# Performance work log

Measured on AMD Instinct MI355X. Metric: run time of the kernel, lower is better.

## Reference

```python
import jax, jax.numpy as jnp
import numpy as np

B, T, C = 32, 4096, 256


def setup_inputs() -> dict:
    key = jax.random.key(0)
    ks = jax.random.split(key, 10)
    s = lambda *sh: 0.05
    return {
        "gru_output": jax.random.normal(ks[0], (B, T, C), jnp.float32),
        "intensity_curves": jax.random.uniform(ks[1], (B, T), jnp.float32),
        "W1": jax.random.normal(ks[2], (C, 128), jnp.float32) * 0.05,
        "b1": jnp.zeros((128,), jnp.float32),
        "W2": jax.random.normal(ks[3], (128, 64), jnp.float32) * 0.05,
        "b2": jnp.zeros((64,), jnp.float32),
        "W3": jax.random.normal(ks[4], (64, 4), jnp.float32) * 0.05,
        "b3": jnp.zeros((4,), jnp.float32),
        "conv_w": jax.random.normal(ks[5], (1, C, 3), jnp.float32) * 0.05,  # OIH
        "conv_b": jnp.zeros((1,), jnp.float32),
    }


def reference(gru_output, intensity_curves, W1, b1, W2, b2, W3, b3, conv_w, conv_b):
    Bb, Tt, Cc = gru_output.shape
    # per-timestep phase classifier MLP + softmax -> (B,T,4)
    h = jax.nn.relu(gru_output @ W1 + b1)
    h = jax.nn.relu(h @ W2 + b2)
    phase_probs = jax.nn.softmax(h @ W3 + b3, axis=-1)
    # transition scores: Conv1d(C->1,k=3,pad=1) + sigmoid -> (B,T)
    x = jnp.transpose(gru_output, (0, 2, 1))  # (B,C,T)
    ts = jax.lax.conv_general_dilated(x, conv_w, (1,), 'SAME',
                                      dimension_numbers=('NCH', 'OIH', 'NCH'))
    transition_scores = jax.nn.sigmoid(ts[:, 0, :] + conv_b[0])  # (B,T)
    # run-length segments: new segment when dominant phase changes or transition>0.7
    dom = jnp.argmax(phase_probs, axis=-1)  # (B,T) int
    change = (dom[:, 1:] != dom[:, :-1]) | (transition_scores[:, 1:] > 0.7)
    change = jnp.concatenate([jnp.zeros((Bb, 1), bool), change], axis=1)
    seg = jnp.cumsum(change.astype(jnp.int32), axis=1)  # (B,T) segment id per step
    gseg = (seg + jnp.arange(Bb, dtype=jnp.int32)[:, None] * Tt).reshape(-1)
    nseg = Bb * Tt
    cnt = jax.ops.segment_sum(jnp.ones((nseg,), jnp.float32)[: gseg.shape[0]] * 0 + 1.0,
                              gseg, num_segments=nseg)
    sum_int = jax.ops.segment_sum(intensity_curves.reshape(-1), gseg, num_segments=nseg)
    conf_t = jnp.take_along_axis(phase_probs, dom[..., None], axis=2)[..., 0]  # (B,T)
    sum_conf = jax.ops.segment_sum(conf_t.reshape(-1), gseg, num_segments=nseg)
    denom = jnp.maximum(cnt, 1.0)
    mean_int = (sum_int / denom)[gseg].reshape(Bb, Tt)   # segment-mean intensity per step
    mean_conf = (sum_conf / denom)[gseg].reshape(Bb, Tt)  # segment-mean confidence per step
    return phase_probs, transition_scores, seg, mean_int, mean_conf
```

## Files before the change

### kernel.cpp

```cpp
#include <hip/hip_runtime.h>

#define B_ 32
#define T_ 4096
#define C_ 256
#define R_ (B_*T_)
#define H1_ 128
#define H2_ 64

#define TB 64

#define PROBS_OFF 0
#define TS_OFF  (R_*4)
#define SEG_OFF (TS_OFF + R_)
#define MI_OFF  (SEG_OFF + R_)
#define MC_OFF  (MI_OFF + R_)

#define XS_OFF  0
#define XS_P    268
#define H1S_OFF 0
#define H1S_P   132
#define W2S_OFF 8448
#define W1S_OFF 17152
#define SMEMF   19200

__device__ __forceinline__ void fma4(float4& a, float s, const float4& b) {
  a.x = fmaf(s, b.x, a.x); a.y = fmaf(s, b.y, a.y);
  a.z = fmaf(s, b.z, a.z); a.w = fmaf(s, b.w, a.w);
}

__global__ __launch_bounds__(256, 2) void mlp_conv_kernel(
    const float* __restrict__ X, const float* __restrict__ W1, const float* __restrict__ b1,
    const float* __restrict__ W2, const float* __restrict__ b2,
    const float* __restrict__ W3, const float* __restrict__ b3,
    const float* __restrict__ CW, const float* __restrict__ CB,
    float* __restrict__ out)
{
  __shared__ float sm[SMEMF];
  const int tid  = threadIdx.x;
  const int l    = tid & 63;
  const int w    = tid >> 6;
  const int row0 = blockIdx.x * TB;

  float4 st0 = ((const float4*)W1)[tid];
  float4 st1 = ((const float4*)W1)[tid + 256];

  #pragma unroll
  for (int i2 = 0; i2 < 16; ++i2) {
    int g = tid + 256 * i2;
    int r = g >> 6, m = g & 63;
    float4 v = *(const float4*)&X[(size_t)(row0 + r) * C_ + m * 4];
    *(float4*)&sm[XS_OFF + r * XS_P + m * 4] = v;
  }
  __syncthreads();

  #pragma unroll
  for (int half = 0; half < 2; ++half) {
    const int rowi = half * 32 + w * 8 + (l & 7);
    const int p = l >> 3;
    const int grow = row0 + rowi;
    const int tb = grow & (T_ - 1);
    float s = 0.f;
    #pragma unroll
    for (int cc = 0; cc < 8; ++cc) {
      const int c = p * 32 + cc * 4;
      float4 x0 = *(const float4*)&sm[XS_OFF + rowi * XS_P + c];
      float4 xm, xp;
      if (tb == 0)             xm = make_float4(0.f, 0.f, 0.f, 0.f);
      else if (rowi >= 1)      xm = *(const float4*)&sm[XS_OFF + (rowi - 1) * XS_P + c];
      else                     xm = *(const float4*)&X[(size_t)(grow - 1) * C_ + c];
      if (tb == T_ - 1)        xp = make_float4(0.f, 0.f, 0.f, 0.f);
      else if (rowi + 1 < TB)  xp = *(const float4*)&sm[XS_OFF + (rowi + 1) * XS_P + c];
      else                     xp = *(const float4*)&X[(size_t)(grow + 1) * C_ + c];
      float4 wa = *(const float4*)&CW[c * 3 + 0];
      float4 wb = *(const float4*)&CW[c * 3 + 4];
      float4 wc = *(const float4*)&CW[c * 3 + 8];
      s += xm.x * wa.x + x0.x * wa.y + xp.x * wa.z;
      s += xm.y * wa.w + x0.y * wb.x + xp.y * wb.y;
      s += xm.z * wb.z + x0.z * wb.w + xp.z * wc.x;
      s += xm.w * wc.y + x0.w * wc.z + xp.w * wc.w;
    }
    s += __shfl_xor(s, 8);
    s += __shfl_xor(s, 16);
    s += __shfl_xor(s, 32);
    if (p == 0) out[TS_OFF + grow] = 1.f / (1.f + expf(-(s + CB[0])));
  }

  const int rt = tid >> 5, ct = tid & 31;
  const int rb = rt * 8;
  float4 acc[8];
  #pragma unroll
  for (int r = 0; r < 8; ++r) acc[r] = make_float4(0.f, 0.f, 0.f, 0.f);

  for (int kc = 0; kc < 16; ++kc) {
    *(float4*)&sm[W1S_OFF + tid * 4]         = st0;
    *(float4*)&sm[W1S_OFF + (tid + 256) * 4] = st1;
    __syncthreads();
    if (kc + 1 < 16) {
      const float* wp = W1 + (size_t)(kc + 1) * 2048;
      st0 = ((const float4*)wp)[tid];
      st1 = ((const float4*)wp)[tid + 256];
    } else {
      st0 = ((const float4*)W2)[tid];
      st1 = ((const float4*)W2)[tid + 256];
    }
    #pragma unroll
    for (int k4 = 0; k4 < 4; ++k4) {
      const int kb = kc * 16 + k4 * 4;
      float4 a0 = *(const float4*)&sm[XS_OFF + (rb + 0) * XS_P + kb];
      float4 a1 = *(const float4*)&sm[XS_OFF + (rb + 1) * XS_P + kb];
      float4 a2 = *(const float4*)&sm[XS_OFF + (rb + 2) * XS_P + kb];
      float4 a3 = *(const float4*)&sm[XS_OFF + (rb + 3) * XS_P + kb];
      float4 a4 = *(const float4*)&sm[XS_OFF + (rb + 4) * XS_P + kb];
      float4 a5 = *(const float4*)&sm[XS_OFF + (rb + 5) * XS_P + kb];
      float4 a6 = *(const float4*)&sm[XS_OFF + (rb + 6) * XS_P + kb];
      float4 a7 = *(const float4*)&sm[XS_OFF + (rb + 7) * XS_P + kb];
      float4 q0 = *(const float4*)&sm[W1S_OFF + (k4 * 4 + 0) * H1_ + ct * 4];
      float4 q1 = *(const float4*)&sm[W1S_OFF + (k4 * 4 + 1) * H1_ + ct * 4];
      float4 q2 = *(const float4*)&sm[W1S_OFF + (k4 * 4 + 2) * H1_ + ct * 4];
      float4 q3 = *(const float4*)&sm[W1S_OFF + (k4 * 4 + 3) * H1_ + ct * 4];
      fma4(acc[0], a0.x, q0); fma4(acc[0], a0.y, q1); fma4(acc[0], a0.z, q2); fma4(acc[0], a0.w, q3);
      fma4(acc[1], a1.x, q0); fma4(acc[1], a1.y, q1); fma4(acc[1], a1.z, q2); fma4(acc[1], a1.w, q3);
      fma4(acc[2], a2.x, q0); fma4(acc[2], a2.y, q1); fma4(acc[2], a2.z, q2); fma4(acc[2], a2.w, q3);
      fma4(acc[3], a3.x, q0); fma4(acc[3], a3.y, q1); fma4(acc[3], a3.z, q2); fma4(acc[3], a3.w, q3);
      fma4(acc[4], a4.x, q0); fma4(acc[4], a4.y, q1); fma4(acc[4], a4.z, q2); fma4(acc[4], a4.w, q3);
      fma4(acc[5], a5.x, q0); fma4(acc[5], a5.y, q1); fma4(acc[5], a5.z, q2); fma4(acc[5], a5.w, q3);
      fma4(acc[6], a6.x, q0); fma4(acc[6], a6.y, q1); fma4(acc[6], a6.z, q2); fma4(acc[6], a6.w, q3);
      fma4(acc[7], a7.x, q0); fma4(acc[7], a7.y, q1); fma4(acc[7], a7.z, q2); fma4(acc[7], a7.w, q3);
    }
    __syncthreads();
  }

  const int rt2 = tid >> 4, ct2 = tid & 15;
  float4 w2r[6];
  #pragma unroll
  for (int i = 0; i < 6; ++i) w2r[i] = ((const float4*)W2)[tid + 512 + 256 * i];
  float4 w30 = ((const float4*)W3)[ct2 * 4 + 0];
  float4 w31 = ((const float4*)W3)[ct2 * 4 + 1];
  float4 w32 = ((const float4*)W3)[ct2 * 4 + 2];
  float4 w33 = ((const float4*)W3)[ct2 * 4 + 3];
  float4 b3v = *(const float4*)&b3[0];

  {
    float4 bb = ((const float4*)b1)[ct];
    #pragma unroll
    for (int r = 0; r < 8; ++r) {
      float4 h = acc[r];
      h.x = fmaxf(h.x + bb.x, 0.f); h.y = fmaxf(h.y + bb.y, 0.f);
      h.z = fmaxf(h.z + bb.z, 0.f); h.w = fmaxf(h.w + bb.w, 0.f);
      *(float4*)&sm[H1S_OFF + (rb + r) * H1S_P + ct * 4] = h;
    }
  }
  *(float4*)&sm[W2S_OFF + tid * 4]         = st0;
  *(float4*)&sm[W2S_OFF + (tid + 256) * 4] = st1;
  #pragma unroll
  for (int i = 0; i < 6; ++i)
    *(float4*)&sm[W2S_OFF + (tid + 512 + 256 * i) * 4] = w2r[i];
  __syncthreads();

  float4 acc2[4];
  #pragma unroll
  for (int j = 0; j < 4; ++j) acc2[j] = make_float4(0.f, 0.f, 0.f, 0.f);
  #pragma unroll 4
  for (int k4 = 0; k4 < 32; ++k4) {
    float4 a0 = *(const float4*)&sm[H1S_OFF + (rt2 * 4 + 0) * H1S_P + k4 * 4];
    float4 a1 = *(const float4*)&sm[H1S_OFF + (rt2 * 4 + 1) * H1S_P + k4 * 4];
    float4 a2 = *(const float4*)&sm[H1S_OFF + (rt2 * 4 + 2) * H1S_P + k4 * 4];
    float4 a3 = *(const float4*)&sm[H1S_OFF + (rt2 * 4 + 3) * H1S_P + k4 * 4];
    float4 q0 = *(const float4*)&sm[W2S_OFF + (k4 * 4 + 0) * H2_ + ct2 * 4];
    float4 q1 = *(const float4*)&sm[W2S_OFF + (k4 * 4 + 1) * H2_ + ct2 * 4];
    float4 q2 = *(const float4*)&sm[W2S_OFF + (k4 * 4 + 2) * H2_ + ct2 * 4];
    float4 q3 = *(const float4*)&sm[W2S_OFF + (k4 * 4 + 3) * H2_ + ct2 * 4];
    fma4(acc2[0], a0.x, q0); fma4(acc2[0], a0.y, q1); fma4(acc2[0], a0.z, q2); fma4(acc2[0], a0.w, q3);
    fma4(acc2[1], a1.x, q0); fma4(acc2[1], a1.y, q1); fma4(acc2[1], a1.z, q2); fma4(acc2[1], a1.w, q3);
    fma4(acc2[2], a2.x, q0); fma4(acc2[2], a2.y, q1); fma4(acc2[2], a2.z, q2); fma4(acc2[2], a2.w, q3);
    fma4(acc2[3], a3.x, q0); fma4(acc2[3], a3.y, q1); fma4(acc2[3], a3.z, q2); fma4(acc2[3], a3.w, q3);
  }

  float4 L[4];
  {
    float4 bb = ((const float4*)b2)[ct2];
    #pragma unroll
    for (int r = 0; r < 4; ++r) {
      float4 h = acc2[r];
      h.x = fmaxf(h.x + bb.x, 0.f); h.y = fmaxf(h.y + bb.y, 0.f);
      h.z = fmaxf(h.z + bb.z, 0.f); h.w = fmaxf(h.w + bb.w, 0.f);
      float4 t = make_float4(0.f, 0.f, 0.f, 0.f);
      fma4(t, h.x, w30); fma4(t, h.y, w31); fma4(t, h.z, w32); fma4(t, h.w, w33);
      L[r] = t;
    }
  }
  #pragma unroll
  for (int d = 1; d < 16; d <<= 1) {
    #pragma unroll
    for (int r = 0; r < 4; ++r) {
      L[r].x += __shfl_xor(L[r].x, d);
      L[r].y += __shfl_xor(L[r].y, d);
      L[r].z += __shfl_xor(L[r].z, d);
      L[r].w += __shfl_xor(L[r].w, d);
    }
  }

  if (ct2 < 4) {
    float4 Lv = L[ct2];
    const int grow = row0 + rt2 * 4 + ct2;
    Lv.x += b3v.x; Lv.y += b3v.y; Lv.z += b3v.z; Lv.w += b3v.w;
    float mx = fmaxf(fmaxf(Lv.x, Lv.y), fmaxf(Lv.z, Lv.w));
    float e0 = expf(Lv.x - mx), e1 = expf(Lv.y - mx), e2 = expf(Lv.z - mx), e3 = expf(Lv.w - mx);
    float inv = 1.f / ((e0 + e1) + (e2 + e3));
    float p0 = e0 * inv, p1 = e1 * inv, p2 = e2 * inv, p3 = e3 * inv;
    *(float4*)&out[PROBS_OFF + (size_t)grow * 4] = make_float4(p0, p1, p2, p3);
    int dom = 0; float pm = p0;
    if (p1 > pm) { pm = p1; dom = 1; }
    if (p2 > pm) { pm = p2; dom = 2; }
    if (p3 > pm) { pm = p3; dom = 3; }
    out[MI_OFF + grow] = (float)dom;
    out[MC_OFF + grow] = pm;
  }
}

__global__ __launch_bounds__(1024, 1) void seg_kernel(
    const float* __restrict__ inten, float* __restrict__ out)
{
  __shared__ float scnt[T_], ssi[T_], ssc[T_];
  __shared__ int wtot[16], wexcl[16];
  const int tid = threadIdx.x;
  const int lane = tid & 63, wid = tid >> 6;
  const size_t base = (size_t)blockIdx.x * T_;
  const float* tsS = out + TS_OFF;
  float* segO = out + SEG_OFF;
  float* miO  = out + MI_OFF;
  float* mcO  = out + MC_OFF;
  const int t4 = tid * 4;

  float4 dv = *(const float4*)&miO[base + t4];
  float4 tv = *(const float4*)&tsS[base + t4];
  float4 iv = *(const float4*)&inten[base + t4];
  float4 cv = *(const float4*)&mcO[base + t4];
  float pd = (tid == 0) ? 0.f : miO[base + t4 - 1];

  for (int i = tid; i < T_; i += 1024) { scnt[i] = 0.f; ssi[i] = 0.f; ssc[i] = 0.f; }

  int c0 = (t4 == 0) ? 0 : (((dv.x != pd)   || (tv.x > 0.7f)) ? 1 : 0);
  int c1 = ((dv.y != dv.x) || (tv.y > 0.7f)) ? 1 : 0;
  int c2 = ((dv.z != dv.y) || (tv.z > 0.7f)) ? 1 : 0;
  int c3 = ((dv.w != dv.z) || (tv.w > 0.7f)) ? 1 : 0;
  int l0 = c0, l1 = c0 + c1, l2 = l1 + c2, l3 = l2 + c3;
  const int tsum = l3;

  int v = tsum;
  #pragma unroll
  for (int d = 1; d < 64; d <<= 1) {
    int o = __shfl_up(v, (unsigned)d);
    if (lane >= d) v += o;
  }
  if (lane == 63) wtot[wid] = v;
  __syncthreads();
  if (tid < 16) {
    int x = wtot[tid];
    int xx = x;
    #pragma unroll
    for (int d = 1; d < 16; d <<= 1) {
      int o = __shfl_up(xx, (unsigned)d);
      if (tid >= d) xx += o;
    }
    wexcl[tid] = xx - x;
  }
  __syncthreads();
  const int texcl = wexcl[wid] + (v - tsum);
  const int s0 = texcl + l0, s1 = texcl + l1, s2 = texcl + l2, s3 = texcl + l3;

  {
    int cur = s0; float aI = iv.x, aC = cv.x, aN = 1.f;
    if (s1 == cur) { aI += iv.y; aC += cv.y; aN += 1.f; }
    else { atomicAdd(&ssi[cur], aI); atomicAdd(&ssc[cur], aC); atomicAdd(&scnt[cur], aN);
           cur = s1; aI = iv.y; aC = cv.y; aN = 1.f; }
    if (s2 == cur) { aI += iv.z; aC += cv.z; aN += 1.f; }
    else { atomicAdd(&ssi[cur], aI); atomicAdd(&ssc[cur], aC); atomicAdd(&scnt[cur], aN);
           cur = s2; aI = iv.z; aC = cv.z; aN = 1.f; }
    if (s3 == cur) { aI += iv.w; aC += cv.w; aN += 1.f; }
    else { atomicAdd(&ssi[cur], aI); atomicAdd(&ssc[cur], aC); atomicAdd(&scnt[cur], aN);
           cur = s3; aI = iv.w; aC = cv.w; aN = 1.f; }
    atomicAdd(&ssi[cur], aI); atomicAdd(&ssc[cur], aC); atomicAdd(&scnt[cur], aN);
  }
  __syncthreads();

  float n0 = scnt[s0], n1 = scnt[s1], n2 = scnt[s2], n3 = scnt[s3];
  float4 m4, q4, g4;
  m4.x = ssi[s0] / n0; m4.y = ssi[s1] / n1; m4.z = ssi[s2] / n2; m4.w = ssi[s3] / n3;
  q4.x = ssc[s0] / n0; q4.y = ssc[s1] / n1; q4.z = ssc[s2] / n2; q4.w = ssc[s3] / n3;
  g4.x = (float)s0; g4.y = (float)s1; g4.z = (float)s2; g4.w = (float)s3;
  *(float4*)&segO[base + t4] = g4;
  *(float4*)&miO[base + t4]  = m4;
  *(float4*)&mcO[base + t4]  = q4;
}

extern "C" void kernel_launch(void* const* d_in, const int* in_sizes, int n_in,
                              void* d_out, int out_size, void* d_ws, size_t ws_size,
                              hipStream_t stream) {
  (void)in_sizes; (void)n_in; (void)out_size; (void)d_ws; (void)ws_size;
  const float* X   = (const float*)d_in[0];
  const float* INT = (const float*)d_in[1];
  const float* W1  = (const float*)d_in[2];
  const float* B1  = (const float*)d_in[3];
  const float* W2  = (const float*)d_in[4];
  const float* B2  = (const float*)d_in[5];
  const float* W3  = (const float*)d_in[6];
  const float* B3  = (const float*)d_in[7];
  const float* CW  = (const float*)d_in[8];
  const float* CB  = (const float*)d_in[9];
  float* out = (float*)d_out;

  hipLaunchKernelGGL(mlp_conv_kernel, dim3(R_ / TB), dim3(256), 0, stream,
                     X, W1, B1, W2, B2, W3, B3, CW, CB, out);
  hipLaunchKernelGGL(seg_kernel, dim3(B_), dim3(1024), 0, stream, INT, out);
}
```

Before: 179.5 us.

## Shrink shared memory by streaming X k-chunks and splitting W2 staging

The full 64-row X tile is no longer held in shared memory for the first GEMM. The conv now stages X in two 32-row halves, and the layer-1 GEMM streams 16-column X chunks into a small padded buffer alongside the W1 chunk, prefetched one step ahead. W2 is staged in two halves with a sync between them, which brings shared memory down from about 77KB to about 50KB, and launch bounds are raised to 3 blocks per CU to increase occupancy. The cost is that each X row is read from global memory twice (once for the conv, once for the GEMM), plus extra barriers and register pressure under the tighter launch bound.

```diff
diff --git a/kernel.cpp b/kernel.cpp
--- a/kernel.cpp
+++ b/kernel.cpp
@@ -16,19 +16,21 @@
 #define MC_OFF  (MI_OFF + R_)
 
 #define XS_OFF  0
-#define XS_P    268
+#define XS_P    260
 #define H1S_OFF 0
 #define H1S_P   132
+#define W1S_OFF 8448
+#define AC_OFF  10496
+#define AC_P    20
 #define W2S_OFF 8448
-#define W1S_OFF 17152
-#define SMEMF   19200
+#define SMEMF   12544
 
 __device__ __forceinline__ void fma4(float4& a, float s, const float4& b) {
   a.x = fmaf(s, b.x, a.x); a.y = fmaf(s, b.y, a.y);
   a.z = fmaf(s, b.z, a.z); a.w = fmaf(s, b.w, a.w);
 }
 
-__global__ __launch_bounds__(256, 2) void mlp_conv_kernel(
+__global__ __launch_bounds__(256, 3) void mlp_conv_kernel(
     const float* __restrict__ X, const float* __restrict__ W1, const float* __restrict__ b1,
     const float* __restrict__ W2, const float* __restrict__ b2,
     const float* __restrict__ W3, const float* __restrict__ b3,
@@ -40,24 +42,26 @@
   const int l    = tid & 63;
   const int w    = tid >> 6;
   const int row0 = blockIdx.x * TB;
+  const float4* Xf4 = (const float4*)X;
 
   float4 st0 = ((const float4*)W1)[tid];
   float4 st1 = ((const float4*)W1)[tid + 256];
-
-  #pragma unroll
-  for (int i2 = 0; i2 < 16; ++i2) {
-    int g = tid + 256 * i2;
-    int r = g >> 6, m = g & 63;
-    float4 v = *(const float4*)&X[(size_t)(row0 + r) * C_ + m * 4];
-    *(float4*)&sm[XS_OFF + r * XS_P + m * 4] = v;
-  }
-  __syncthreads();
+  float4 sa0 = Xf4[(size_t)(row0 + (tid >> 2)) * 64 + (tid & 3)];
 
   #pragma unroll
   for (int half = 0; half < 2; ++half) {
-    const int rowi = half * 32 + w * 8 + (l & 7);
+    if (half) __syncthreads();
+    #pragma unroll
+    for (int i2 = 0; i2 < 8; ++i2) {
+      int g = tid + 256 * i2;
+      int r = g >> 6, m = g & 63;
+      float4 v = *(const float4*)&X[(size_t)(row0 + half * 32 + r) * C_ + m * 4];
+      *(float4*)&sm[XS_OFF + r * XS_P + m * 4] = v;
+    }
+    __syncthreads();
+    const int rowi = w * 8 + (l & 7);
     const int p = l >> 3;
-    const int grow = row0 + rowi;
+    const int grow = row0 + half * 32 + rowi;
     const int tb = grow & (T_ - 1);
     float s = 0.f;
     #pragma unroll
@@ -65,12 +69,12 @@
       const int c = p * 32 + cc * 4;
       float4 x0 = *(const float4*)&sm[XS_OFF + rowi * XS_P + c];
       float4 xm, xp;
-      if (tb == 0)             xm = make_float4(0.f, 0.f, 0.f, 0.f);
-      else if (rowi >= 1)      xm = *(const float4*)&sm[XS_OFF + (rowi - 1) * XS_P + c];
-      else                     xm = *(const float4*)&X[(size_t)(grow - 1) * C_ + c];
-      if (tb == T_ - 1)        xp = make_float4(0.f, 0.f, 0.f, 0.f);
-      else if (rowi + 1 < TB)  xp = *(const float4*)&sm[XS_OFF + (rowi + 1) * XS_P + c];
-      else                     xp = *(const float4*)&X[(size_t)(grow + 1) * C_ + c];
+      if (tb == 0)            xm = make_float4(0.f, 0.f, 0.f, 0.f);
+      else if (rowi >= 1)     xm = *(const float4*)&sm[XS_OFF + (rowi - 1) * XS_P + c];
+      else                    xm = *(const float4*)&X[(size_t)(grow - 1) * C_ + c];
+      if (tb == T_ - 1)       xp = make_float4(0.f, 0.f, 0.f, 0.f);
+      else if (rowi + 1 < 32) xp = *(const float4*)&sm[XS_OFF + (rowi + 1) * XS_P + c];
+      else                    xp = *(const float4*)&X[(size_t)(grow + 1) * C_ + c];
       float4 wa = *(const float4*)&CW[c * 3 + 0];
       float4 wb = *(const float4*)&CW[c * 3 + 4];
       float4 wc = *(const float4*)&CW[c * 3 + 8];
@@ -84,9 +88,12 @@
     s += __shfl_xor(s, 32);
     if (p == 0) out[TS_OFF + grow] = 1.f / (1.f + expf(-(s + CB[0])));
   }
+  __syncthreads();
 
   const int rt = tid >> 5, ct = tid & 31;
   const int rb = rt * 8;
+  const int acq = (tid >> 2) * AC_P + (tid & 3) * 4;
+  float4 w2x;
   float4 acc[8];
   #pragma unroll
   for (int r = 0; r < 8; ++r) acc[r] = make_float4(0.f, 0.f, 0.f, 0.f);
@@ -94,26 +101,29 @@
   for (int kc = 0; kc < 16; ++kc) {
     *(float4*)&sm[W1S_OFF + tid * 4]         = st0;
     *(float4*)&sm[W1S_OFF + (tid + 256) * 4] = st1;
+    *(float4*)&sm[AC_OFF + acq]              = sa0;
     __syncthreads();
     if (kc + 1 < 16) {
       const float* wp = W1 + (size_t)(kc + 1) * 2048;
       st0 = ((const float4*)wp)[tid];
       st1 = ((const float4*)wp)[tid + 256];
+      sa0 = Xf4[(size_t)(row0 + (tid >> 2)) * 64 + (kc + 1) * 4 + (tid & 3)];
     } else {
       st0 = ((const float4*)W2)[tid];
       st1 = ((const float4*)W2)[tid + 256];
+      sa0 = ((const float4*)W2)[tid + 512];
+      w2x = ((const float4*)W2)[tid + 768];
     }
     #pragma unroll
     for (int k4 = 0; k4 < 4; ++k4) {
-      const int kb = kc * 16 + k4 * 4;
-      float4 a0 = *(const float4*)&sm[XS_OFF + (rb + 0) * XS_P + kb];
-      float4 a1 = *(const float4*)&sm[XS_OFF + (rb + 1) * XS_P + kb];
-      float4 a2 = *(const float4*)&sm[XS_OFF + (rb + 2) * XS_P + kb];
-      float4 a3 = *(const float4*)&sm[XS_OFF + (rb + 3) * XS_P + kb];
-      float4 a4 = *(const float4*)&sm[XS_OFF + (rb + 4) * XS_P + kb];
-      float4 a5 = *(const float4*)&sm[XS_OFF + (rb + 5) * XS_P + kb];
-      float4 a6 = *(const float4*)&sm[XS_OFF + (rb + 6) * XS_P + kb];
-      float4 a7 = *(const float4*)&sm[XS_OFF + (rb + 7) * XS_P + kb];
+      float4 a0 = *(const float4*)&sm[AC_OFF + (rb + 0) * AC_P + k4 * 4];
+      float4 a1 = *(const float4*)&sm[AC_OFF + (rb + 1) * AC_P + k4 * 4];
+      float4 a2 = *(const float4*)&sm[AC_OFF + (rb + 2) * AC_P + k4 * 4];
+      float4 a3 = *(const float4*)&sm[AC_OFF + (rb + 3) * AC_P + k4 * 4];
+      float4 a4 = *(const float4*)&sm[AC_OFF + (rb + 4) * AC_P + k4 * 4];
+      float4 a5 = *(const float4*)&sm[AC_OFF + (rb + 5) * AC_P + k4 * 4];
+      float4 a6 = *(const float4*)&sm[AC_OFF + (rb + 6) * AC_P + k4 * 4];
+      float4 a7 = *(const float4*)&sm[AC_OFF + (rb + 7) * AC_P + k4 * 4];
       float4 q0 = *(const float4*)&sm[W1S_OFF + (k4 * 4 + 0) * H1_ + ct * 4];
       float4 q1 = *(const float4*)&sm[W1S_OFF + (k4 * 4 + 1) * H1_ + ct * 4];
       float4 q2 = *(const float4*)&sm[W1S_OFF + (k4 * 4 + 2) * H1_ + ct * 4];
@@ -131,9 +141,6 @@
   }
 
   const int rt2 = tid >> 4, ct2 = tid & 15;
-  float4 w2r[6];
-  #pragma unroll
-  for (int i = 0; i < 6; ++i) w2r[i] = ((const float4*)W2)[tid + 512 + 256 * i];
   float4 w30 = ((const float4*)W3)[ct2 * 4 + 0];
   float4 w31 = ((const float4*)W3)[ct2 * 4 + 1];
   float4 w32 = ((const float4*)W3)[ct2 * 4 + 2];
@@ -152,16 +159,20 @@
   }
   *(float4*)&sm[W2S_OFF + tid * 4]         = st0;
   *(float4*)&sm[W2S_OFF + (tid + 256) * 4] = st1;
-  #pragma unroll
-  for (int i = 0; i < 6; ++i)
-    *(float4*)&sm[W2S_OFF + (tid + 512 + 256 * i) * 4] = w2r[i];
-  __syncthreads();
+  *(float4*)&sm[W2S_OFF + (tid + 512) * 4] = sa0;
+  *(float4*)&sm[W2S_OFF + (tid + 768) * 4] = w2x;
+  __syncthreads();
+
+  st0 = ((const float4*)W2)[tid + 1024];
+  st1 = ((const float4*)W2)[tid + 1280];
+  sa0 = ((const float4*)W2)[tid + 1536];
+  w2x = ((const float4*)W2)[tid + 1792];
 
   float4 acc2[4];
   #pragma unroll
   for (int j = 0; j < 4; ++j) acc2[j] = make_float4(0.f, 0.f, 0.f, 0.f);
   #pragma unroll 4
-  for (int k4 = 0; k4 < 32; ++k4) {
+  for (int k4 = 0; k4 < 16; ++k4) {
     float4 a0 = *(const float4*)&sm[H1S_OFF + (rt2 * 4 + 0) * H1S_P + k4 * 4];
     float4 a1 = *(const float4*)&sm[H1S_OFF + (rt2 * 4 + 1) * H1S_P + k4 * 4];
     float4 a2 = *(const float4*)&sm[H1S_OFF + (rt2 * 4 + 2) * H1S_P + k4 * 4];
@@ -170,6 +181,27 @@
     float4 q1 = *(const float4*)&sm[W2S_OFF + (k4 * 4 + 1) * H2_ + ct2 * 4];
     float4 q2 = *(const float4*)&sm[W2S_OFF + (k4 * 4 + 2) * H2_ + ct2 * 4];
     float4 q3 = *(const float4*)&sm[W2S_OFF + (k4 * 4 + 3) * H2_ + ct2 * 4];
+    fma4(acc2[0], a0.x, q0); fma4(acc2[0], a0.y, q1); fma4(acc2[0], a0.z, q2); fma4(acc2[0], a0.w, q3);
+    fma4(acc2[1], a1.x, q0); fma4(acc2[1], a1.y, q1); fma4(acc2[1], a1.z, q2); fma4(acc2[1], a1.w, q3);
+    fma4(acc2[2], a2.x, q0); fma4(acc2[2], a2.y, q1); fma4(acc2[2], a2.z, q2); fma4(acc2[2], a2.w, q3);
+    fma4(acc2[3], a3.x, q0); fma4(acc2[3], a3.y, q1); fma4(acc2[3], a3.z, q2); fma4(acc2[3], a3.w, q3);
+  }
+  __syncthreads();
+  *(float4*)&sm[W2S_OFF + tid * 4]         = st0;
+  *(float4*)&sm[W2S_OFF + (tid + 256) * 4] = st1;
+  *(float4*)&sm[W2S_OFF + (tid + 512) * 4] = sa0;
+  *(float4*)&sm[W2S_OFF + (tid + 768) * 4] = w2x;
+  __syncthreads();
+  #pragma unroll 4
+  for (int k4 = 16; k4 < 32; ++k4) {
+    float4 a0 = *(const float4*)&sm[H1S_OFF + (rt2 * 4 + 0) * H1S_P + k4 * 4];
+    float4 a1 = *(const float4*)&sm[H1S_OFF + (rt2 * 4 + 1) * H1S_P + k4 * 4];
+    float4 a2 = *(const float4*)&sm[H1S_OFF + (rt2 * 4 + 2) * H1S_P + k4 * 4];
+    float4 a3 = *(const float4*)&sm[H1S_OFF + (rt2 * 4 + 3) * H1S_P + k4 * 4];
+    float4 q0 = *(const float4*)&sm[W2S_OFF + ((k4 - 16) * 4 + 0) * H2_ + ct2 * 4];
+    float4 q1 = *(const float4*)&sm[W2S_OFF + ((k4 - 16) * 4 + 1) * H2_ + ct2 * 4];
+    float4 q2 = *(const float4*)&sm[W2S_OFF + ((k4 - 16) * 4 + 2) * H2_ + ct2 * 4];
+    float4 q3 = *(const float4*)&sm[W2S_OFF + ((k4 - 16) * 4 + 3) * H2_ + ct2 * 4];
     fma4(acc2[0], a0.x, q0); fma4(acc2[0], a0.y, q1); fma4(acc2[0], a0.z, q2); fma4(acc2[0], a0.w, q3);
     fma4(acc2[1], a1.x, q0); fma4(acc2[1], a1.y, q1); fma4(acc2[1], a1.z, q2); fma4(acc2[1], a1.w, q3);
     fma4(acc2[2], a2.x, q0); fma4(acc2[2], a2.y, q1); fma4(acc2[2], a2.z, q2); fma4(acc2[2], a2.w, q3);
```

New measurement: 231.1 us. +28.7%, slower.

## Drop LDS staging of X and weights; stream operands from global with register double-buffering

Applied to the files above, without the earlier changes.

The kernel no longer stages the X tile and the W1/W2 weight chunks through shared memory. The conv and the first GEMM read X directly from global memory, and both GEMMs read weights straight from global/L2 with software-pipelined register double buffers. Only the hidden activations H1 stay in LDS. This shrinks LDS use and removes most barriers, and launch bounds are raised to 3 blocks per CU for more occupancy. The cost is redundant global/L2 traffic: each X row is re-read by many threads and weights are fetched per thread, so it relies on cache hit rates and may pressure registers under the tighter bound.

```diff
diff --git a/kernel.cpp b/kernel.cpp
--- a/kernel.cpp
+++ b/kernel.cpp
@@ -15,20 +15,15 @@
 #define MI_OFF  (SEG_OFF + R_)
 #define MC_OFF  (MI_OFF + R_)
 
-#define XS_OFF  0
-#define XS_P    268
-#define H1S_OFF 0
 #define H1S_P   132
-#define W2S_OFF 8448
-#define W1S_OFF 17152
-#define SMEMF   19200
+#define SMEMF   (64 * H1S_P)
 
 __device__ __forceinline__ void fma4(float4& a, float s, const float4& b) {
   a.x = fmaf(s, b.x, a.x); a.y = fmaf(s, b.y, a.y);
   a.z = fmaf(s, b.z, a.z); a.w = fmaf(s, b.w, a.w);
 }
 
-__global__ __launch_bounds__(256, 2) void mlp_conv_kernel(
+__global__ __launch_bounds__(256, 3) void mlp_conv_kernel(
     const float* __restrict__ X, const float* __restrict__ W1, const float* __restrict__ b1,
     const float* __restrict__ W2, const float* __restrict__ b2,
     const float* __restrict__ W3, const float* __restrict__ b3,
@@ -41,36 +36,23 @@
   const int w    = tid >> 6;
   const int row0 = blockIdx.x * TB;
 
-  float4 st0 = ((const float4*)W1)[tid];
-  float4 st1 = ((const float4*)W1)[tid + 256];
-
-  #pragma unroll
-  for (int i2 = 0; i2 < 16; ++i2) {
-    int g = tid + 256 * i2;
-    int r = g >> 6, m = g & 63;
-    float4 v = *(const float4*)&X[(size_t)(row0 + r) * C_ + m * 4];
-    *(float4*)&sm[XS_OFF + r * XS_P + m * 4] = v;
-  }
-  __syncthreads();
-
   #pragma unroll
   for (int half = 0; half < 2; ++half) {
     const int rowi = half * 32 + w * 8 + (l & 7);
     const int p = l >> 3;
     const int grow = row0 + rowi;
     const int tb = grow & (T_ - 1);
+    const float* x0p = X + (size_t)grow * C_;
     float s = 0.f;
     #pragma unroll
     for (int cc = 0; cc < 8; ++cc) {
       const int c = p * 32 + cc * 4;
-      float4 x0 = *(const float4*)&sm[XS_OFF + rowi * XS_P + c];
+      float4 x0 = *(const float4*)&x0p[c];
       float4 xm, xp;
-      if (tb == 0)             xm = make_float4(0.f, 0.f, 0.f, 0.f);
-      else if (rowi >= 1)      xm = *(const float4*)&sm[XS_OFF + (rowi - 1) * XS_P + c];
-      else                     xm = *(const float4*)&X[(size_t)(grow - 1) * C_ + c];
-      if (tb == T_ - 1)        xp = make_float4(0.f, 0.f, 0.f, 0.f);
-      else if (rowi + 1 < TB)  xp = *(const float4*)&sm[XS_OFF + (rowi + 1) * XS_P + c];
-      else                     xp = *(const float4*)&X[(size_t)(grow + 1) * C_ + c];
+      if (tb == 0)        xm = make_float4(0.f, 0.f, 0.f, 0.f);
+      else                xm = *(const float4*)&x0p[c - C_];
+      if (tb == T_ - 1)   xp = make_float4(0.f, 0.f, 0.f, 0.f);
+      else                xp = *(const float4*)&x0p[c + C_];
       float4 wa = *(const float4*)&CW[c * 3 + 0];
       float4 wb = *(const float4*)&CW[c * 3 + 4];
       float4 wc = *(const float4*)&CW[c * 3 + 8];
@@ -87,103 +69,99 @@
 
   const int rt = tid >> 5, ct = tid & 31;
   const int rb = rt * 8;
+  const float* xb = X + (size_t)(row0 + rb) * C_;
+  const float* wb1 = W1 + ct * 4;
   float4 acc[8];
   #pragma unroll
   for (int r = 0; r < 8; ++r) acc[r] = make_float4(0.f, 0.f, 0.f, 0.f);
-
-  for (int kc = 0; kc < 16; ++kc) {
-    *(float4*)&sm[W1S_OFF + tid * 4]         = st0;
-    *(float4*)&sm[W1S_OFF + (tid + 256) * 4] = st1;
-    __syncthreads();
-    if (kc + 1 < 16) {
-      const float* wp = W1 + (size_t)(kc + 1) * 2048;
-      st0 = ((const float4*)wp)[tid];
-      st1 = ((const float4*)wp)[tid + 256];
-    } else {
-      st0 = ((const float4*)W2)[tid];
-      st1 = ((const float4*)W2)[tid + 256];
-    }
-    #pragma unroll
-    for (int k4 = 0; k4 < 4; ++k4) {
-      const int kb = kc * 16 + k4 * 4;
-      float4 a0 = *(const float4*)&sm[XS_OFF + (rb + 0) * XS_P + kb];
-      float4 a1 = *(const float4*)&sm[XS_OFF + (rb + 1) * XS_P + kb];
-      float4 a2 = *(const float4*)&sm[XS_OFF + (rb + 2) * XS_P + kb];
-      float4 a3 = *(const float4*)&sm[XS_OFF + (rb + 3) * XS_P + kb];
-      float4 a4 = *(const float4*)&sm[XS_OFF + (rb + 4) * XS_P + kb];
-      float4 a5 = *(const float4*)&sm[XS_OFF + (rb + 5) * XS_P + kb];
-      float4 a6 = *(const float4*)&sm[XS_OFF + (rb + 6) * XS_P + kb];
-      float4 a7 = *(const float4*)&sm[XS_OFF + (rb + 7) * XS_P + kb];
-      float4 q0 = *(const float4*)&sm[W1S_OFF + (k4 * 4 + 0) * H1_ + ct * 4];
-      float4 q1 = *(const float4*)&sm[W1S_OFF + (k4 * 4 + 1) * H1_ + ct * 4];
-      float4 q2 = *(const float4*)&sm[W1S_OFF + (k4 * 4 + 2) * H1_ + ct * 4];
-      float4 q3 = *(const float4*)&sm[W1S_OFF + (k4 * 4 + 3) * H1_ + ct * 4];
-      fma4(acc[0], a0.x, q0); fma4(acc[0], a0.y, q1); fma4(acc[0], a0.z, q2); fma4(acc[0], a0.w, q3);
-      fma4(acc[1], a1.x, q0); fma4(acc[1], a1.y, q1); fma4(acc[1], a1.z, q2); fma4(acc[1], a1.w, q3);
-      fma4(acc[2], a2.x, q0); fma4(acc[2], a2.y, q1); fma4(acc[2], a2.z, q2); fma4(acc[2], a2.w, q3);
-      fma4(acc[3], a3.x, q0); fma4(acc[3], a3.y, q1); fma4(acc[3], a3.z, q2); fma4(acc[3], a3.w, q3);
-      fma4(acc[4], a4.x, q0); fma4(acc[4], a4.y, q1); fma4(acc[4], a4.z, q2); fma4(acc[4], a4.w, q3);
-      fma4(acc[5], a5.x, q0); fma4(acc[5], a5.y, q1); fma4(acc[5], a5.z, q2); fma4(acc[5], a5.w, q3);
-      fma4(acc[6], a6.x, q0); fma4(acc[6], a6.y, q1); fma4(acc[6], a6.z, q2); fma4(acc[6], a6.w, q3);
-      fma4(acc[7], a7.x, q0); fma4(acc[7], a7.y, q1); fma4(acc[7], a7.z, q2); fma4(acc[7], a7.w, q3);
-    }
-    __syncthreads();
-  }
+  {
+    float4 A0[8], A1[8], B0[4], B1[4];
+    #pragma unroll
+    for (int r = 0; r < 8; ++r) A0[r] = *(const float4*)&xb[r * C_];
+    #pragma unroll
+    for (int j = 0; j < 4; ++j) B0[j] = *(const float4*)&wb1[(size_t)j * H1_];
+
+    #define G1STEP(Ac, Bc, An, Bn, kb, pf)                                        \
+      {                                                                           \
+        if (pf) {                                                                 \
+          _Pragma("unroll")                                                       \
+          for (int r = 0; r < 8; ++r) An[r] = *(const float4*)&xb[r * C_ + (kb) + 4]; \
+          _Pragma("unroll")                                                       \
+          for (int j = 0; j < 4; ++j) Bn[j] = *(const float4*)&wb1[(size_t)((kb) + 4 + j) * H1_]; \
+        }                                                                         \
+        _Pragma("unroll")                                                         \
+        for (int r = 0; r < 8; ++r) {                                             \
+          fma4(acc[r], Ac[r].x, Bc[0]); fma4(acc[r], Ac[r].y, Bc[1]);             \
+          fma4(acc[r], Ac[r].z, Bc[2]); fma4(acc[r], Ac[r].w, Bc[3]);             \
+        }                                                                         \
+      }
+
+    for (int k4 = 0; k4 < 64; k4 += 2) {
+      G1STEP(A0, B0, A1, B1, k4 * 4, 1)
+      G1STEP(A1, B1, A0, B0, k4 * 4 + 4, (k4 + 2 < 64))
+    }
+    #undef G1STEP
+  }
+
+  {
+    float4 bb = ((const float4*)b1)[ct];
+    #pragma unroll
+    for (int r = 0; r < 8; ++r) {
+      float4 h = acc[r];
+      h.x = fmaxf(h.x + bb.x, 0.f); h.y = fmaxf(h.y + bb.y, 0.f);
+      h.z = fmaxf(h.z + bb.z, 0.f); h.w = fmaxf(h.w + bb.w, 0.f);
+      *(float4*)&sm[(rb + r) * H1S_P + ct * 4] = h;
+    }
+  }
+  __syncthreads();
 
   const int rt2 = tid >> 4, ct2 = tid & 15;
-  float4 w2r[6];
-  #pragma unroll
-  for (int i = 0; i < 6; ++i) w2r[i] = ((const float4*)W2)[tid + 512 + 256 * i];
   float4 w30 = ((const float4*)W3)[ct2 * 4 + 0];
   float4 w31 = ((const float4*)W3)[ct2 * 4 + 1];
   float4 w32 = ((const float4*)W3)[ct2 * 4 + 2];
   float4 w33 = ((const float4*)W3)[ct2 * 4 + 3];
+  float4 b2v = ((const float4*)b2)[ct2];
   float4 b3v = *(const float4*)&b3[0];
-
-  {
-    float4 bb = ((const float4*)b1)[ct];
-    #pragma unroll
-    for (int r = 0; r < 8; ++r) {
-      float4 h = acc[r];
-      h.x = fmaxf(h.x + bb.x, 0.f); h.y = fmaxf(h.y + bb.y, 0.f);
-      h.z = fmaxf(h.z + bb.z, 0.f); h.w = fmaxf(h.w + bb.w, 0.f);
-      *(float4*)&sm[H1S_OFF + (rb + r) * H1S_P + ct * 4] = h;
-    }
-  }
-  *(float4*)&sm[W2S_OFF + tid * 4]         = st0;
-  *(float4*)&sm[W2S_OFF + (tid + 256) * 4] = st1;
-  #pragma unroll
-  for (int i = 0; i < 6; ++i)
-    *(float4*)&sm[W2S_OFF + (tid + 512 + 256 * i) * 4] = w2r[i];
-  __syncthreads();
-
+  const float* w2b = W2 + ct2 * 4;
   float4 acc2[4];
   #pragma unroll
   for (int j = 0; j < 4; ++j) acc2[j] = make_float4(0.f, 0.f, 0.f, 0.f);
-  #pragma unroll 4
-  for (int k4 = 0; k4 < 32; ++k4) {
-    float4 a0 = *(const float4*)&sm[H1S_OFF + (rt2 * 4 + 0) * H1S_P + k4 * 4];
-    float4 a1 = *(const float4*)&sm[H1S_OFF + (rt2 * 4 + 1) * H1S_P + k4 * 4];
-    float4 a2 = *(const float4*)&sm[H1S_OFF + (rt2 * 4 + 2) * H1S_P + k4 * 4];
-    float4 a3 = *(const float4*)&sm[H1S_OFF + (rt2 * 4 + 3) * H1S_P + k4 * 4];
-    float4 q0 = *(const float4*)&sm[W2S_OFF + (k4 * 4 + 0) * H2_ + ct2 * 4];
-    float4 q1 = *(const float4*)&sm[W2S_OFF + (k4 * 4 + 1) * H2_ + ct2 * 4];
-    float4 q2 = *(const float4*)&sm[W2S_OFF + (k4 * 4 + 2) * H2_ + ct2 * 4];
-    float4 q3 = *(const float4*)&sm[W2S_OFF + (k4 * 4 + 3) * H2_ + ct2 * 4];
-    fma4(acc2[0], a0.x, q0); fma4(acc2[0], a0.y, q1); fma4(acc2[0], a0.z, q2); fma4(acc2[0], a0.w, q3);
-    fma4(acc2[1], a1.x, q0); fma4(acc2[1], a1.y, q1); fma4(acc2[1], a1.z, q2); fma4(acc2[1], a1.w, q3);
-    fma4(acc2[2], a2.x, q0); fma4(acc2[2], a2.y, q1); fma4(acc2[2], a2.z, q2); fma4(acc2[2], a2.w, q3);
-    fma4(acc2[3], a3.x, q0); fma4(acc2[3], a3.y, q1); fma4(acc2[3], a3.z, q2); fma4(acc2[3], a3.w, q3);
+  {
+    float4 A0[4], A1[4], B0[4], B1[4];
+    #pragma unroll
+    for (int r = 0; r < 4; ++r) A0[r] = *(const float4*)&sm[(rt2 * 4 + r) * H1S_P];
+    #pragma unroll
+    for (int j = 0; j < 4; ++j) B0[j] = *(const float4*)&w2b[(size_t)j * H2_];
+
+    #define G2STEP(Ac, Bc, An, Bn, kb, pf)                                        \
+      {                                                                           \
+        if (pf) {                                                                 \
+          _Pragma("unroll")                                                       \
+          for (int r = 0; r < 4; ++r) An[r] = *(const float4*)&sm[(rt2 * 4 + r) * H1S_P + (kb) + 4]; \
+          _Pragma("unroll")                                                       \
+          for (int j = 0; j < 4; ++j) Bn[j] = *(const float4*)&w2b[(size_t)((kb) + 4 + j) * H2_]; \
+        }                                                                         \
+        _Pragma("unroll")                                                         \
+        for (int r = 0; r < 4; ++r) {                                             \
+          fma4(acc2[r], Ac[r].x, Bc[0]); fma4(acc2[r], Ac[r].y, Bc[1]);           \
+          fma4(acc2[r], Ac[r].z, Bc[2]); fma4(acc2[r], Ac[r].w, Bc[3]);           \
+        }                                                                         \
+      }
+
+    for (int k4 = 0; k4 < 32; k4 += 2) {
+      G2STEP(A0, B0, A1, B1, k4 * 4, 1)
+      G2STEP(A1, B1, A0, B0, k4 * 4 + 4, (k4 + 2 < 32))
+    }
+    #undef G2STEP
   }
 
   float4 L[4];
   {
-    float4 bb = ((const float4*)b2)[ct2];
     #pragma unroll
     for (int r = 0; r < 4; ++r) {
       float4 h = acc2[r];
-      h.x = fmaxf(h.x + bb.x, 0.f); h.y = fmaxf(h.y + bb.y, 0.f);
-      h.z = fmaxf(h.z + bb.z, 0.f); h.w = fmaxf(h.w + bb.w, 0.f);
+      h.x = fmaxf(h.x + b2v.x, 0.f); h.y = fmaxf(h.y + b2v.y, 0.f);
+      h.z = fmaxf(h.z + b2v.z, 0.f); h.w = fmaxf(h.w + b2v.w, 0.f);
       float4 t = make_float4(0.f, 0.f, 0.f, 0.f);
       fma4(t, h.x, w30); fma4(t, h.y, w31); fma4(t, h.z, w32); fma4(t, h.w, w33);
       L[r] = t;
```

Measured after the change: 511.4 us, median of 2. +184.8%, slower.

## Double-buffer W1 chunks in LDS to halve barriers in first GEMM

Applied to the files above, without the earlier changes.

Replaces the single W1 staging buffer, which took two barriers per 16-row chunk, with two 8-row ping-pong buffers that are written while the other is being consumed, so each 8-row chunk needs one barrier. The first W1 chunk is stored before the conv stage so it overlaps that work. The X tile row pitch is also reduced from 268 to 260 floats, which changes the LDS bank pattern. W2 staging is moved entirely after the GEMM loop. Smaller chunks mean more loop iterations and possibly different bank conflicts in the X reads.

```diff
diff --git a/kernel.cpp b/kernel.cpp
--- a/kernel.cpp
+++ b/kernel.cpp
@@ -16,17 +16,44 @@
 #define MC_OFF  (MI_OFF + R_)
 
 #define XS_OFF  0
-#define XS_P    268
+#define XS_P    260
 #define H1S_OFF 0
 #define H1S_P   132
 #define W2S_OFF 8448
-#define W1S_OFF 17152
-#define SMEMF   19200
+#define W1B0    16640
+#define W1B1    17664
+#define SMEMF   18688
 
 __device__ __forceinline__ void fma4(float4& a, float s, const float4& b) {
   a.x = fmaf(s, b.x, a.x); a.y = fmaf(s, b.y, a.y);
   a.z = fmaf(s, b.z, a.z); a.w = fmaf(s, b.w, a.w);
 }
+
+#define G1CHUNK(BOFF, CB)                                                      \
+  _Pragma("unroll")                                                            \
+  for (int k4 = 0; k4 < 2; ++k4) {                                            \
+    const int colb = (CB) + k4 * 4;                                           \
+    float4 a0 = *(const float4*)&sm[XS_OFF + (rb + 0) * XS_P + colb];         \
+    float4 a1 = *(const float4*)&sm[XS_OFF + (rb + 1) * XS_P + colb];         \
+    float4 a2 = *(const float4*)&sm[XS_OFF + (rb + 2) * XS_P + colb];         \
+    float4 a3 = *(const float4*)&sm[XS_OFF + (rb + 3) * XS_P + colb];         \
+    float4 a4 = *(const float4*)&sm[XS_OFF + (rb + 4) * XS_P + colb];         \
+    float4 a5 = *(const float4*)&sm[XS_OFF + (rb + 5) * XS_P + colb];         \
+    float4 a6 = *(const float4*)&sm[XS_OFF + (rb + 6) * XS_P + colb];         \
+    float4 a7 = *(const float4*)&sm[XS_OFF + (rb + 7) * XS_P + colb];         \
+    float4 q0 = *(const float4*)&sm[(BOFF) + (k4 * 4 + 0) * H1_ + ct * 4];    \
+    float4 q1 = *(const float4*)&sm[(BOFF) + (k4 * 4 + 1) * H1_ + ct * 4];    \
+    float4 q2 = *(const float4*)&sm[(BOFF) + (k4 * 4 + 2) * H1_ + ct * 4];    \
+    float4 q3 = *(const float4*)&sm[(BOFF) + (k4 * 4 + 3) * H1_ + ct * 4];    \
+    fma4(acc[0], a0.x, q0); fma4(acc[0], a0.y, q1); fma4(acc[0], a0.z, q2); fma4(acc[0], a0.w, q3); \
+    fma4(acc[1], a1.x, q0); fma4(acc[1], a1.y, q1); fma4(acc[1], a1.z, q2); fma4(acc[1], a1.w, q3); \
+    fma4(acc[2], a2.x, q0); fma4(acc[2], a2.y, q1); fma4(acc[2], a2.z, q2); fma4(acc[2], a2.w, q3); \
+    fma4(acc[3], a3.x, q0); fma4(acc[3], a3.y, q1); fma4(acc[3], a3.z, q2); fma4(acc[3], a3.w, q3); \
+    fma4(acc[4], a4.x, q0); fma4(acc[4], a4.y, q1); fma4(acc[4], a4.z, q2); fma4(acc[4], a4.w, q3); \
+    fma4(acc[5], a5.x, q0); fma4(acc[5], a5.y, q1); fma4(acc[5], a5.z, q2); fma4(acc[5], a5.w, q3); \
+    fma4(acc[6], a6.x, q0); fma4(acc[6], a6.y, q1); fma4(acc[6], a6.z, q2); fma4(acc[6], a6.w, q3); \
+    fma4(acc[7], a7.x, q0); fma4(acc[7], a7.y, q1); fma4(acc[7], a7.z, q2); fma4(acc[7], a7.w, q3); \
+  }
 
 __global__ __launch_bounds__(256, 2) void mlp_conv_kernel(
     const float* __restrict__ X, const float* __restrict__ W1, const float* __restrict__ b1,
@@ -41,8 +68,7 @@
   const int w    = tid >> 6;
   const int row0 = blockIdx.x * TB;
 
-  float4 st0 = ((const float4*)W1)[tid];
-  float4 st1 = ((const float4*)W1)[tid + 256];
+  float4 st = ((const float4*)W1)[tid];
 
   #pragma unroll
   for (int i2 = 0; i2 < 16; ++i2) {
@@ -52,6 +78,9 @@
     *(float4*)&sm[XS_OFF + r * XS_P + m * 4] = v;
   }
   __syncthreads();
+
+  *(float4*)&sm[W1B0 + tid * 4] = st;
+  st = ((const float4*)W1)[256 + tid];
 
   #pragma unroll
   for (int half = 0; half < 2; ++half) {
@@ -84,6 +113,7 @@
     s += __shfl_xor(s, 32);
     if (p == 0) out[TS_OFF + grow] = 1.f / (1.f + expf(-(s + CB[0])));
   }
+  __syncthreads();
 
   const int rt = tid >> 5, ct = tid & 31;
   const int rb = rt * 8;
@@ -91,53 +121,29 @@
   #pragma unroll
   for (int r = 0; r < 8; ++r) acc[r] = make_float4(0.f, 0.f, 0.f, 0.f);
 
-  for (int kc = 0; kc < 16; ++kc) {
-    *(float4*)&sm[W1S_OFF + tid * 4]         = st0;
-    *(float4*)&sm[W1S_OFF + (tid + 256) * 4] = st1;
+  #pragma unroll 1
+  for (int c = 0; c < 32; c += 2) {
+    G1CHUNK(W1B0, c * 8)
+    *(float4*)&sm[W1B1 + tid * 4] = st;
+    if (c + 2 < 32) st = ((const float4*)W1)[(c + 2) * 256 + tid];
     __syncthreads();
-    if (kc + 1 < 16) {
-      const float* wp = W1 + (size_t)(kc + 1) * 2048;
-      st0 = ((const float4*)wp)[tid];
-      st1 = ((const float4*)wp)[tid + 256];
-    } else {
-      st0 = ((const float4*)W2)[tid];
-      st1 = ((const float4*)W2)[tid + 256];
-    }
-    #pragma unroll
-    for (int k4 = 0; k4 < 4; ++k4) {
-      const int kb = kc * 16 + k4 * 4;
-      float4 a0 = *(const float4*)&sm[XS_OFF + (rb + 0) * XS_P + kb];
-      float4 a1 = *(const float4*)&sm[XS_OFF + (rb + 1) * XS_P + kb];
-      float4 a2 = *(const float4*)&sm[XS_OFF + (rb + 2) * XS_P + kb];
-      float4 a3 = *(const float4*)&sm[XS_OFF + (rb + 3) * XS_P + kb];
-      float4 a4 = *(const float4*)&sm[XS_OFF + (rb + 4) * XS_P + kb];
-      float4 a5 = *(const float4*)&sm[XS_OFF + (rb + 5) * XS_P + kb];
-      float4 a6 = *(const float4*)&sm[XS_OFF + (rb + 6) * XS_P + kb];
-      float4 a7 = *(const float4*)&sm[XS_OFF + (rb + 7) * XS_P + kb];
-      float4 q0 = *(const float4*)&sm[W1S_OFF + (k4 * 4 + 0) * H1_ + ct * 4];
-      float4 q1 = *(const float4*)&sm[W1S_OFF + (k4 * 4 + 1) * H1_ + ct * 4];
-      float4 q2 = *(const float4*)&sm[W1S_OFF + (k4 * 4 + 2) * H1_ + ct * 4];
-      float4 q3 = *(const float4*)&sm[W1S_OFF + (k4 * 4 + 3) * H1_ + ct * 4];
-      fma4(acc[0], a0.x, q0); fma4(acc[0], a0.y, q1); fma4(acc[0], a0.z, q2); fma4(acc[0], a0.w, q3);
-      fma4(acc[1], a1.x, q0); fma4(acc[1], a1.y, q1); fma4(acc[1], a1.z, q2); fma4(acc[1], a1.w, q3);
-      fma4(acc[2], a2.x, q0); fma4(acc[2], a2.y, q1); fma4(acc[2], a2.z, q2); fma4(acc[2], a2.w, q3);
-      fma4(acc[3], a3.x, q0); fma4(acc[3], a3.y, q1); fma4(acc[3], a3.z, q2); fma4(acc[3], a3.w, q3);
-      fma4(acc[4], a4.x, q0); fma4(acc[4], a4.y, q1); fma4(acc[4], a4.z, q2); fma4(acc[4], a4.w, q3);
-      fma4(acc[5], a5.x, q0); fma4(acc[5], a5.y, q1); fma4(acc[5], a5.z, q2); fma4(acc[5], a5.w, q3);
-      fma4(acc[6], a6.x, q0); fma4(acc[6], a6.y, q1); fma4(acc[6], a6.z, q2); fma4(acc[6], a6.w, q3);
-      fma4(acc[7], a7.x, q0); fma4(acc[7], a7.y, q1); fma4(acc[7], a7.z, q2); fma4(acc[7], a7.w, q3);
+    G1CHUNK(W1B1, c * 8 + 8)
+    if (c + 2 < 32) {
+      *(float4*)&sm[W1B0 + tid * 4] = st;
+      st = ((const float4*)W1)[(c + 3) * 256 + tid];
     }
     __syncthreads();
   }
 
   const int rt2 = tid >> 4, ct2 = tid & 15;
-  float4 w2r[6];
-  #pragma unroll
-  for (int i = 0; i < 6; ++i) w2r[i] = ((const float4*)W2)[tid + 512 + 256 * i];
+  float4 w2q[8];
+  #pragma unroll
+  for (int i = 0; i < 8; ++i) w2q[i] = ((const float4*)W2)[tid + 256 * i];
   float4 w30 = ((const float4*)W3)[ct2 * 4 + 0];
   float4 w31 = ((const float4*)W3)[ct2 * 4 + 1];
   float4 w32 = ((const float4*)W3)[ct2 * 4 + 2];
   float4 w33 = ((const float4*)W3)[ct2 * 4 + 3];
+  float4 b2v = ((const float4*)b2)[ct2];
   float4 b3v = *(const float4*)&b3[0];
 
   {
@@ -150,11 +156,9 @@
       *(float4*)&sm[H1S_OFF + (rb + r) * H1S_P + ct * 4] = h;
     }
   }
-  *(float4*)&sm[W2S_OFF + tid * 4]         = st0;
-  *(float4*)&sm[W2S_OFF + (tid + 256) * 4] = st1;
-  #pragma unroll
-  for (int i = 0; i < 6; ++i)
-    *(float4*)&sm[W2S_OFF + (tid + 512 + 256 * i) * 4] = w2r[i];
+  #pragma unroll
+  for (int i = 0; i < 8; ++i)
+    *(float4*)&sm[W2S_OFF + (tid + 256 * i) * 4] = w2q[i];
   __syncthreads();
 
   float4 acc2[4];
@@ -178,12 +182,11 @@
 
   float4 L[4];
   {
-    float4 bb = ((const float4*)b2)[ct2];
     #pragma unroll
     for (int r = 0; r < 4; ++r) {
       float4 h = acc2[r];
-      h.x = fmaxf(h.x + bb.x, 0.f); h.y = fmaxf(h.y + bb.y, 0.f);
-      h.z = fmaxf(h.z + bb.z, 0.f); h.w = fmaxf(h.w + bb.w, 0.f);
+      h.x = fmaxf(h.x + b2v.x, 0.f); h.y = fmaxf(h.y + b2v.y, 0.f);
+      h.z = fmaxf(h.z + b2v.z, 0.f); h.w = fmaxf(h.w + b2v.w, 0.f);
       float4 t = make_float4(0.f, 0.f, 0.f, 0.f);
       fma4(t, h.x, w30); fma4(t, h.y, w31); fma4(t, h.z, w32); fma4(t, h.w, w33);
       L[r] = t;
```

Measured after the change: 202.8 us. +13.0%, slower.
